# Kernel optimization log

Measured on AMD Instinct MI355X. Metric: run time of the kernel, lower is better.

## Reference

```python
import jax, jax.numpy as jnp
import numpy as np

B, S, D, H = 4, 2048, 1024, 16


def setup_inputs() -> dict:
    key = jax.random.key(0)
    ks = jax.random.split(key, 5)
    scale = 1.0 / np.sqrt(D)
    return {
        "q": jax.random.normal(ks[0], (B, S, D), jnp.float32),
        "v": jax.random.normal(ks[1], (B, S, D), jnp.float32),
        "Wq": jax.random.normal(ks[2], (D, D), jnp.float32) * scale,
        "bq": jnp.zeros((D,), jnp.float32),
        "Wk": jax.random.normal(ks[3], (D, D), jnp.float32) * scale,
        "bk": jnp.zeros((D,), jnp.float32),
        "Wv": jax.random.normal(ks[4], (D, D), jnp.float32) * scale,
        "bv": jnp.zeros((D,), jnp.float32),
    }


def reference(q, v, Wq, bq, Wk, bk, Wv, bv):
    # k defaults to v in the original call
    k = v
    embed_dim = Wq.shape[0]
    num_heads = H
    dh = embed_dim // num_heads
    b, s, _ = q.shape

    qp = q @ Wq + bq  # [B,S,D]
    kp = k @ Wk + bk
    vp = v @ Wv + bv

    # tf.split(x, H, axis=2) + concat on axis 0 == reshape to [B,S,H,dh]
    qh = qp.reshape(b, s, num_heads, dh)
    kh = kp.reshape(b, s, num_heads, dh)
    vh = vp.reshape(b, s, num_heads, dh)

    # NOTE: original scales by sqrt(embed_dim), NOT sqrt(head_dim)
    scores = jnp.einsum("bqhd,bkhd->bhqk", qh, kh) / jnp.sqrt(
        jnp.asarray(embed_dim, qh.dtype)
    )
    att = jax.nn.softmax(scores, axis=-1)
    out = jnp.einsum("bhqk,bkhd->bqhd", att, vh)
    return out.reshape(b, s, embed_dim)
```

## Files before the change

kernel.cpp:

```cpp
#include <hip/hip_runtime.h>
#include <hip/hip_bf16.h>
#include <math.h>

#define B_   4
#define S_   2048
#define D_   1024
#define H_   16
#define DH_  64
#define M_   (B_ * S_)
#define BH_  (B_ * H_)

typedef __bf16 bf16x8_t __attribute__((ext_vector_type(8)));
typedef float  f32x4_t  __attribute__((ext_vector_type(4)));
typedef float  f32x16_t __attribute__((ext_vector_type(16)));

#define QSCALE 0.045084220027780106f

__device__ __forceinline__ unsigned short f2bf(float x) {
  unsigned int u = __float_as_uint(x);
  u += 0x7fffu + ((u >> 16) & 1u);
  return (unsigned short)(u >> 16);
}

__device__ __forceinline__ unsigned int pk2t(float lo, float hi) {
  return __builtin_amdgcn_perm(__float_as_uint(hi), __float_as_uint(lo), 0x07060302u);
}

__device__ __forceinline__ void async16(const void* g, void* l) {
  __builtin_amdgcn_global_load_lds(
      (__attribute__((address_space(1))) unsigned int*)(void*)g,
      (__attribute__((address_space(3))) unsigned int*)l, 16, 0, 0);
}

__global__ __launch_bounds__(256) void cvt_f32_bf16(
    const float* __restrict__ q, const float* __restrict__ v,
    unsigned short* __restrict__ qb, unsigned short* __restrict__ vb) {
  const float* src = blockIdx.y ? v : q;
  unsigned short* dst = blockIdx.y ? vb : qb;
  size_t i = ((size_t)blockIdx.x * 256 + threadIdx.x) * 4;
  float4 a = *(const float4*)(src + i);
  ushort4 o;
  o.x = f2bf(a.x); o.y = f2bf(a.y); o.z = f2bf(a.z); o.w = f2bf(a.w);
  *(ushort4*)(dst + i) = o;
}

__global__ void wtrans(const float* __restrict__ Wq, const float* __restrict__ Wk,
                       const float* __restrict__ Wv,
                       unsigned short* __restrict__ Wqt, unsigned short* __restrict__ Wkt,
                       unsigned short* __restrict__ Wvt) {
  int z = blockIdx.z;
  const float* W = (z == 0) ? Wq : (z == 1 ? Wk : Wv);
  unsigned short* Wt = (z == 0) ? Wqt : (z == 1 ? Wkt : Wvt);
  __shared__ float tile[32][33];
  int tx = threadIdx.x, ty = threadIdx.y;
  int n = blockIdx.x * 32 + tx;
#pragma unroll
  for (int i = 0; i < 4; ++i) {
    int k = blockIdx.y * 32 + ty + i * 8;
    tile[ty + i * 8][tx] = W[(size_t)k * D_ + n];
  }
  __syncthreads();
  int k2 = blockIdx.y * 32 + tx;
#pragma unroll
  for (int i = 0; i < 4; ++i) {
    int n2 = blockIdx.x * 32 + ty + i * 8;
    Wt[(size_t)n2 * D_ + k2] = f2bf(tile[tx][ty + i * 8]);
  }
}

__global__ __launch_bounds__(256) void proj_gemm(
    const unsigned short* __restrict__ Aq, const unsigned short* __restrict__ Av,
    const unsigned short* __restrict__ Wqt, const unsigned short* __restrict__ Wkt,
    const unsigned short* __restrict__ Wvt,
    const float* __restrict__ bq, const float* __restrict__ bk, const float* __restrict__ bv,
    unsigned short* __restrict__ qp, unsigned short* __restrict__ kp,
    unsigned short* __restrict__ vt) {
  int z = blockIdx.y;
  const unsigned short* A  = (z == 0) ? Aq : Av;
  const unsigned short* Wt = (z == 0) ? Wqt : (z == 1 ? Wkt : Wvt);
  const float* bias        = (z == 0) ? bq : (z == 1 ? bk : bv);
  unsigned short* outp     = (z == 0) ? qp : (z == 1 ? kp : vt);
  const float cs           = (z == 0) ? QSCALE : 1.0f;

  int lin = blockIdx.x;
  int xcd = lin & 7, j = lin >> 3;
  int m0 = (xcd * 8 + (j & 7)) * 128;
  int n0 = (j >> 3) * 128;

  __shared__ __attribute__((aligned(16))) unsigned short Alds[128 * 32];
  __shared__ __attribute__((aligned(16))) unsigned short Blds[128 * 32];

  int t = threadIdx.x;
  int lane = t & 63, wave = t >> 6;
  int lrow = lane & 15, lq = lane >> 4;
  int wm = (wave & 1) * 64, wn = (wave >> 1) * 64;

  f32x4_t acc[4][4];
#pragma unroll
  for (int i = 0; i < 4; ++i)
#pragma unroll
    for (int j2 = 0; j2 < 4; ++j2) acc[i][j2] = (f32x4_t){0.f, 0.f, 0.f, 0.f};

  for (int k0 = 0; k0 < D_; k0 += 32) {
    __syncthreads();
#pragma unroll
    for (int r = 0; r < 2; ++r) {
      int off = t * 16 + r * 4096;
      int row = off >> 6, slot = (off >> 4) & 3;
      int ch = (slot ^ (row >> 1)) & 3;
      async16((const char*)A  + ((size_t)(m0 + row) * D_ + k0) * 2 + ch * 16, (char*)Alds + off);
      async16((const char*)Wt + ((size_t)(n0 + row) * D_ + k0) * 2 + ch * 16, (char*)Blds + off);
    }
    __syncthreads();

    bf16x8_t af[4], bfr[4];
#pragma unroll
    for (int i = 0; i < 4; ++i) {
      int ra = wm + i * 16 + lrow;
      int rb = wn + i * 16 + lrow;
      af[i]  = *(const bf16x8_t*)(Alds + ra * 32 + ((lq ^ (ra >> 1)) & 3) * 8);
      bfr[i] = *(const bf16x8_t*)(Blds + rb * 32 + ((lq ^ (rb >> 1)) & 3) * 8);
    }
#pragma unroll
    for (int i = 0; i < 4; ++i)
#pragma unroll
      for (int j2 = 0; j2 < 4; ++j2)
        acc[i][j2] = __builtin_amdgcn_mfma_f32_16x16x32_bf16(af[i], bfr[j2], acc[i][j2], 0, 0, 0);
  }

#pragma unroll
  for (int j2 = 0; j2 < 4; ++j2) {
    int n = n0 + wn + j2 * 16 + lrow;
    float bv_ = bias[n];
    int h = n >> 6, d = n & 63;
#pragma unroll
    for (int i = 0; i < 4; ++i) {
      int mbase = m0 + wm + i * 16 + lq * 4;
      int b = mbase >> 11, s = mbase & 2047;
      if (z != 2) {
#pragma unroll
        for (int r = 0; r < 4; ++r)
          outp[(((size_t)(b * H_ + h) * S_ + (s + r)) << 6) + d] = f2bf((acc[i][j2][r] + bv_) * cs);
      } else {
        ushort4 pk;
        pk.x = f2bf(acc[i][j2][0] + bv_);
        pk.y = f2bf(acc[i][j2][1] + bv_);
        pk.z = f2bf(acc[i][j2][2] + bv_);
        pk.w = f2bf(acc[i][j2][3] + bv_);
        *(ushort4*)(outp + (((size_t)(b * H_ + h) * 64 + d) << 11) + s) = pk;
      }
    }
  }
}

__global__ __launch_bounds__(256, 2) void attn(
    const unsigned short* __restrict__ qp, const unsigned short* __restrict__ kp,
    const unsigned short* __restrict__ vt, float* __restrict__ out) {
  const int bh = blockIdx.x;
  const int qt = blockIdx.y;
  const int t = threadIdx.x;
  const int lane = t & 63, wave = t >> 6;
  const int h = lane >> 5, ln = lane & 31;

  __shared__ __attribute__((aligned(16))) unsigned short Klds[2][64 * 64];
  __shared__ __attribute__((aligned(16))) unsigned short Vlds[2][64 * 64];

  const int q0 = qt * 256 + wave * 64;

  bf16x8_t qf[2][4];
#pragma unroll
  for (int rt = 0; rt < 2; ++rt)
#pragma unroll
    for (int ks = 0; ks < 4; ++ks)
      qf[rt][ks] = *(const bf16x8_t*)(qp + ((size_t)bh * S_ + q0 + rt * 32 + ln) * 64 + ks * 16 + h * 8);

  f32x16_t o[2][2];
  float l[2] = {0.f, 0.f};
#pragma unroll
  for (int rt = 0; rt < 2; ++rt)
#pragma unroll
    for (int dt = 0; dt < 2; ++dt)
#pragma unroll
      for (int r = 0; r < 16; ++r) o[rt][dt][r] = 0.f;

  f32x16_t z16;
#pragma unroll
  for (int r = 0; r < 16; ++r) z16[r] = 0.f;

  const unsigned short* kg = kp + (size_t)bh * S_ * 64;
  const unsigned short* vg = vt + (size_t)bh * 64 * S_;

  auto stage = [&](int kb, int bi) {
#pragma unroll
    for (int r = 0; r < 2; ++r) {
      int off = t * 16 + r * 4096;
      int row = off >> 7, slot = (off >> 4) & 7;
      int ch = slot ^ (row & 7);
      async16((const char*)(kg + (size_t)(kb + row) * 64 + ch * 8), (char*)&Klds[bi][0] + off);
      async16((const char*)(vg + (size_t)row * S_ + kb + ch * 8), (char*)&Vlds[bi][0] + off);
    }
  };

  stage(0, 0);

  const int NT = S_ / 64;
  for (int it = 0; it < NT; ++it) {
    const int bi = it & 1;
    __syncthreads();
    if (it + 1 < NT) stage((it + 1) * 64, bi ^ 1);

    const unsigned short* Kb = &Klds[bi][0];
    const unsigned short* Vb = &Vlds[bi][0];

    f32x16_t st[2][2];
#pragma unroll
    for (int kt = 0; kt < 2; ++kt) {
      {
        int row = kt * 32 + ln;
        bf16x8_t kf = *(const bf16x8_t*)(Kb + row * 64 + (((0 + h) ^ (row & 7)) * 8));
        st[0][kt] = __builtin_amdgcn_mfma_f32_32x32x16_bf16(kf, qf[0][0], z16, 0, 0, 0);
        st[1][kt] = __builtin_amdgcn_mfma_f32_32x32x16_bf16(kf, qf[1][0], z16, 0, 0, 0);
      }
#pragma unroll
      for (int ks = 1; ks < 4; ++ks) {
        int row = kt * 32 + ln;
        bf16x8_t kf = *(const bf16x8_t*)(Kb + row * 64 + (((ks * 2 + h) ^ (row & 7)) * 8));
        st[0][kt] = __builtin_amdgcn_mfma_f32_32x32x16_bf16(kf, qf[0][ks], st[0][kt], 0, 0, 0);
        st[1][kt] = __builtin_amdgcn_mfma_f32_32x32x16_bf16(kf, qf[1][ks], st[1][kt], 0, 0, 0);
      }
    }

    unsigned int pkv[2][2][8];
#pragma unroll
    for (int rt = 0; rt < 2; ++rt) {
      float lp = 0.f;
#pragma unroll
      for (int kt = 0; kt < 2; ++kt)
#pragma unroll
        for (int i = 0; i < 8; ++i) {
          float p0 = __builtin_amdgcn_exp2f(st[rt][kt][2 * i]);
          float p1 = __builtin_amdgcn_exp2f(st[rt][kt][2 * i + 1]);
          lp += p0 + p1;
          pkv[rt][kt][i] = pk2t(p0, p1);
        }
      l[rt] += lp + __shfl_xor(lp, 32);
    }

    bf16x8_t pf[2][4];
#pragma unroll
    for (int rt = 0; rt < 2; ++rt)
#pragma unroll
      for (int ks = 0; ks < 4; ++ks) {
        int kt = ks >> 1, b = 4 * (ks & 1);
        unsigned int e0 = __shfl_xor(h ? pkv[rt][kt][b]     : pkv[rt][kt][b + 2], 32);
        unsigned int e1 = __shfl_xor(h ? pkv[rt][kt][b + 1] : pkv[rt][kt][b + 3], 32);
        union { unsigned int u[4]; bf16x8_t v; } fr;
        fr.u[0] = h ? e0 : pkv[rt][kt][b];
        fr.u[1] = h ? e1 : pkv[rt][kt][b + 1];
        fr.u[2] = h ? pkv[rt][kt][b + 2] : e0;
        fr.u[3] = h ? pkv[rt][kt][b + 3] : e1;
        pf[rt][ks] = fr.v;
      }

#pragma unroll
    for (int dt = 0; dt < 2; ++dt)
#pragma unroll
      for (int ks = 0; ks < 4; ++ks) {
        int row = dt * 32 + ln;
        bf16x8_t vf = *(const bf16x8_t*)(Vb + row * 64 + (((ks * 2 + h) ^ (row & 7)) * 8));
#pragma unroll
        for (int rt = 0; rt < 2; ++rt)
          o[rt][dt] = __builtin_amdgcn_mfma_f32_32x32x16_bf16(pf[rt][ks], vf, o[rt][dt], 0, 0, 0);
      }
  }

  const int b = bh >> 4, head = bh & 15;
#pragma unroll
  for (int rt = 0; rt < 2; ++rt)
#pragma unroll
    for (int r = 0; r < 16; ++r) {
      int rowl = (r & 3) + 8 * (r >> 2) + 4 * h;
      float li = __shfl(l[rt], rowl, 64);
      float inv = __builtin_amdgcn_rcpf(li);
      int rg = q0 + rt * 32 + rowl;
      float* op = out + ((size_t)b * S_ + rg) * D_ + head * 64 + ln;
      op[0]  = o[rt][0][r] * inv;
      op[32] = o[rt][1][r] * inv;
    }
}

extern "C" void kernel_launch(void* const* d_in, const int* in_sizes, int n_in,
                              void* d_out, int out_size, void* d_ws, size_t ws_size,
                              hipStream_t stream) {
  const float* q  = (const float*)d_in[0];
  const float* v  = (const float*)d_in[1];
  const float* Wq = (const float*)d_in[2];
  const float* bq = (const float*)d_in[3];
  const float* Wk = (const float*)d_in[4];
  const float* bk = (const float*)d_in[5];
  const float* Wv = (const float*)d_in[6];
  const float* bv = (const float*)d_in[7];
  float* out = (float*)d_out;

  char* ws = (char*)d_ws;
  unsigned short* qb  = (unsigned short*)(ws);
  unsigned short* vb  = (unsigned short*)(ws + (16u << 20));
  unsigned short* Wqt = (unsigned short*)(ws + (32u << 20));
  unsigned short* Wkt = (unsigned short*)(ws + (34u << 20));
  unsigned short* Wvt = (unsigned short*)(ws + (36u << 20));
  unsigned short* qpp = (unsigned short*)(ws + (38u << 20));
  unsigned short* kpp = (unsigned short*)(ws + (54u << 20));
  unsigned short* vtp = (unsigned short*)(ws + (70u << 20));

  hipLaunchKernelGGL(cvt_f32_bf16, dim3((M_ * D_) / 1024, 2), dim3(256), 0, stream,
                     q, v, qb, vb);
  hipLaunchKernelGGL(wtrans, dim3(32, 32, 3), dim3(32, 8), 0, stream,
                     Wq, Wk, Wv, Wqt, Wkt, Wvt);
  hipLaunchKernelGGL(proj_gemm, dim3(512, 3), dim3(256), 0, stream,
                     qb, vb, Wqt, Wkt, Wvt, bq, bk, bv, qpp, kpp, vtp);
  hipLaunchKernelGGL(attn, dim3(BH_, S_ / 256), dim3(256), 0, stream,
                     qpp, kpp, vtp, out);
}
```

Baseline: 274.3 us.

## Deepen projection GEMM K-tile, shrink attention query tile, compute row sums via MFMA

The projection GEMM now stages 64-wide K slices with an 8-chunk XOR swizzle, which halves the number of barrier-separated loop iterations. The attention kernel drops from 64 to 32 query rows per wave and doubles the grid. It raises launch bounds to 4 blocks per CU so more waves can hide latency. The softmax denominator now comes from an extra MFMA against a ones vector instead of scalar adds and shuffles. This adds MFMA work and halves K/V reuse per staged tile, trading that for lower register pressure and higher occupancy.

```diff
diff --git a/kernel.cpp b/kernel.cpp
--- a/kernel.cpp
+++ b/kernel.cpp
@@ -87,8 +87,8 @@
   int m0 = (xcd * 8 + (j & 7)) * 128;
   int n0 = (j >> 3) * 128;
 
-  __shared__ __attribute__((aligned(16))) unsigned short Alds[128 * 32];
-  __shared__ __attribute__((aligned(16))) unsigned short Blds[128 * 32];
+  __shared__ __attribute__((aligned(16))) unsigned short Alds[128 * 64];
+  __shared__ __attribute__((aligned(16))) unsigned short Blds[128 * 64];
 
   int t = threadIdx.x;
   int lane = t & 63, wave = t >> 6;
@@ -101,31 +101,34 @@
 #pragma unroll
     for (int j2 = 0; j2 < 4; ++j2) acc[i][j2] = (f32x4_t){0.f, 0.f, 0.f, 0.f};
 
-  for (int k0 = 0; k0 < D_; k0 += 32) {
+  for (int k0 = 0; k0 < D_; k0 += 64) {
     __syncthreads();
 #pragma unroll
-    for (int r = 0; r < 2; ++r) {
+    for (int r = 0; r < 4; ++r) {
       int off = t * 16 + r * 4096;
-      int row = off >> 6, slot = (off >> 4) & 3;
-      int ch = (slot ^ (row >> 1)) & 3;
+      int row = off >> 7, slot = (off >> 4) & 7;
+      int ch = slot ^ (row & 7);
       async16((const char*)A  + ((size_t)(m0 + row) * D_ + k0) * 2 + ch * 16, (char*)Alds + off);
       async16((const char*)Wt + ((size_t)(n0 + row) * D_ + k0) * 2 + ch * 16, (char*)Blds + off);
     }
     __syncthreads();
 
-    bf16x8_t af[4], bfr[4];
-#pragma unroll
-    for (int i = 0; i < 4; ++i) {
-      int ra = wm + i * 16 + lrow;
-      int rb = wn + i * 16 + lrow;
-      af[i]  = *(const bf16x8_t*)(Alds + ra * 32 + ((lq ^ (ra >> 1)) & 3) * 8);
-      bfr[i] = *(const bf16x8_t*)(Blds + rb * 32 + ((lq ^ (rb >> 1)) & 3) * 8);
-    }
-#pragma unroll
-    for (int i = 0; i < 4; ++i)
-#pragma unroll
-      for (int j2 = 0; j2 < 4; ++j2)
-        acc[i][j2] = __builtin_amdgcn_mfma_f32_16x16x32_bf16(af[i], bfr[j2], acc[i][j2], 0, 0, 0);
+#pragma unroll
+    for (int kk = 0; kk < 2; ++kk) {
+      bf16x8_t af[4], bfr[4];
+#pragma unroll
+      for (int i = 0; i < 4; ++i) {
+        int ra = wm + i * 16 + lrow;
+        int rb = wn + i * 16 + lrow;
+        af[i]  = *(const bf16x8_t*)((const char*)Alds + ra * 128 + (((lq + 4 * kk) ^ (ra & 7)) * 16));
+        bfr[i] = *(const bf16x8_t*)((const char*)Blds + rb * 128 + (((lq + 4 * kk) ^ (rb & 7)) * 16));
+      }
+#pragma unroll
+      for (int i = 0; i < 4; ++i)
+#pragma unroll
+        for (int j2 = 0; j2 < 4; ++j2)
+          acc[i][j2] = __builtin_amdgcn_mfma_f32_16x16x32_bf16(af[i], bfr[j2], acc[i][j2], 0, 0, 0);
+    }
   }
 
 #pragma unroll
@@ -153,7 +156,7 @@
   }
 }
 
-__global__ __launch_bounds__(256, 2) void attn(
+__global__ __launch_bounds__(256, 4) void attn(
     const unsigned short* __restrict__ qp, const unsigned short* __restrict__ kp,
     const unsigned short* __restrict__ vt, float* __restrict__ out) {
   const int bh = blockIdx.x;
@@ -165,27 +168,25 @@
   __shared__ __attribute__((aligned(16))) unsigned short Klds[2][64 * 64];
   __shared__ __attribute__((aligned(16))) unsigned short Vlds[2][64 * 64];
 
-  const int q0 = qt * 256 + wave * 64;
-
-  bf16x8_t qf[2][4];
-#pragma unroll
-  for (int rt = 0; rt < 2; ++rt)
-#pragma unroll
-    for (int ks = 0; ks < 4; ++ks)
-      qf[rt][ks] = *(const bf16x8_t*)(qp + ((size_t)bh * S_ + q0 + rt * 32 + ln) * 64 + ks * 16 + h * 8);
-
-  f32x16_t o[2][2];
-  float l[2] = {0.f, 0.f};
-#pragma unroll
-  for (int rt = 0; rt < 2; ++rt)
-#pragma unroll
-    for (int dt = 0; dt < 2; ++dt)
-#pragma unroll
-      for (int r = 0; r < 16; ++r) o[rt][dt][r] = 0.f;
+  const int q0 = qt * 128 + wave * 32;
+
+  bf16x8_t qf[4];
+#pragma unroll
+  for (int ks = 0; ks < 4; ++ks)
+    qf[ks] = *(const bf16x8_t*)(qp + ((size_t)bh * S_ + q0 + ln) * 64 + ks * 16 + h * 8);
+
+  f32x16_t o[2];
+  f32x16_t o_l;
+#pragma unroll
+  for (int r = 0; r < 16; ++r) { o[0][r] = 0.f; o[1][r] = 0.f; o_l[r] = 0.f; }
 
   f32x16_t z16;
 #pragma unroll
   for (int r = 0; r < 16; ++r) z16[r] = 0.f;
+
+  bf16x8_t onesf;
+#pragma unroll
+  for (int i = 0; i < 8; ++i) onesf[i] = (__bf16)1.0f;
 
   const unsigned short* kg = kp + (size_t)bh * S_ * 64;
   const unsigned short* vg = vt + (size_t)bh * 64 * S_;
@@ -212,81 +213,70 @@
     const unsigned short* Kb = &Klds[bi][0];
     const unsigned short* Vb = &Vlds[bi][0];
 
-    f32x16_t st[2][2];
+    f32x16_t st[2];
 #pragma unroll
     for (int kt = 0; kt < 2; ++kt) {
+      int row = kt * 32 + ln;
       {
-        int row = kt * 32 + ln;
-        bf16x8_t kf = *(const bf16x8_t*)(Kb + row * 64 + (((0 + h) ^ (row & 7)) * 8));
-        st[0][kt] = __builtin_amdgcn_mfma_f32_32x32x16_bf16(kf, qf[0][0], z16, 0, 0, 0);
-        st[1][kt] = __builtin_amdgcn_mfma_f32_32x32x16_bf16(kf, qf[1][0], z16, 0, 0, 0);
+        bf16x8_t kf = *(const bf16x8_t*)(Kb + row * 64 + ((h ^ (row & 7)) * 8));
+        st[kt] = __builtin_amdgcn_mfma_f32_32x32x16_bf16(kf, qf[0], z16, 0, 0, 0);
       }
 #pragma unroll
       for (int ks = 1; ks < 4; ++ks) {
-        int row = kt * 32 + ln;
         bf16x8_t kf = *(const bf16x8_t*)(Kb + row * 64 + (((ks * 2 + h) ^ (row & 7)) * 8));
-        st[0][kt] = __builtin_amdgcn_mfma_f32_32x32x16_bf16(kf, qf[0][ks], st[0][kt], 0, 0, 0);
-        st[1][kt] = __builtin_amdgcn_mfma_f32_32x32x16_bf16(kf, qf[1][ks], st[1][kt], 0, 0, 0);
-      }
-    }
-
-    unsigned int pkv[2][2][8];
-#pragma unroll
-    for (int rt = 0; rt < 2; ++rt) {
-      float lp = 0.f;
-#pragma unroll
-      for (int kt = 0; kt < 2; ++kt)
-#pragma unroll
-        for (int i = 0; i < 8; ++i) {
-          float p0 = __builtin_amdgcn_exp2f(st[rt][kt][2 * i]);
-          float p1 = __builtin_amdgcn_exp2f(st[rt][kt][2 * i + 1]);
-          lp += p0 + p1;
-          pkv[rt][kt][i] = pk2t(p0, p1);
-        }
-      l[rt] += lp + __shfl_xor(lp, 32);
-    }
-
-    bf16x8_t pf[2][4];
-#pragma unroll
-    for (int rt = 0; rt < 2; ++rt)
+        st[kt] = __builtin_amdgcn_mfma_f32_32x32x16_bf16(kf, qf[ks], st[kt], 0, 0, 0);
+      }
+    }
+
+    unsigned int pkv[2][8];
+#pragma unroll
+    for (int kt = 0; kt < 2; ++kt)
+#pragma unroll
+      for (int i = 0; i < 8; ++i) {
+        float p0 = __builtin_amdgcn_exp2f(st[kt][2 * i]);
+        float p1 = __builtin_amdgcn_exp2f(st[kt][2 * i + 1]);
+        pkv[kt][i] = pk2t(p0, p1);
+      }
+
+    bf16x8_t pf[4];
+#pragma unroll
+    for (int ks = 0; ks < 4; ++ks) {
+      int kt = ks >> 1, b = 4 * (ks & 1);
+      unsigned int e0 = __shfl_xor(h ? pkv[kt][b]     : pkv[kt][b + 2], 32);
+      unsigned int e1 = __shfl_xor(h ? pkv[kt][b + 1] : pkv[kt][b + 3], 32);
+      union { unsigned int u[4]; bf16x8_t v; } fr;
+      fr.u[0] = h ? e0 : pkv[kt][b];
+      fr.u[1] = h ? e1 : pkv[kt][b + 1];
+      fr.u[2] = h ? pkv[kt][b + 2] : e0;
+      fr.u[3] = h ? pkv[kt][b + 3] : e1;
+      pf[ks] = fr.v;
+    }
+
+#pragma unroll
+    for (int ks = 0; ks < 4; ++ks)
+      o_l = __builtin_amdgcn_mfma_f32_32x32x16_bf16(pf[ks], onesf, o_l, 0, 0, 0);
+
+#pragma unroll
+    for (int dt = 0; dt < 2; ++dt) {
+      int row = dt * 32 + ln;
 #pragma unroll
       for (int ks = 0; ks < 4; ++ks) {
-        int kt = ks >> 1, b = 4 * (ks & 1);
-        unsigned int e0 = __shfl_xor(h ? pkv[rt][kt][b]     : pkv[rt][kt][b + 2], 32);
-        unsigned int e1 = __shfl_xor(h ? pkv[rt][kt][b + 1] : pkv[rt][kt][b + 3], 32);
-        union { unsigned int u[4]; bf16x8_t v; } fr;
-        fr.u[0] = h ? e0 : pkv[rt][kt][b];
-        fr.u[1] = h ? e1 : pkv[rt][kt][b + 1];
-        fr.u[2] = h ? pkv[rt][kt][b + 2] : e0;
-        fr.u[3] = h ? pkv[rt][kt][b + 3] : e1;
-        pf[rt][ks] = fr.v;
-      }
-
-#pragma unroll
-    for (int dt = 0; dt < 2; ++dt)
-#pragma unroll
-      for (int ks = 0; ks < 4; ++ks) {
-        int row = dt * 32 + ln;
         bf16x8_t vf = *(const bf16x8_t*)(Vb + row * 64 + (((ks * 2 + h) ^ (row & 7)) * 8));
-#pragma unroll
-        for (int rt = 0; rt < 2; ++rt)
-          o[rt][dt] = __builtin_amdgcn_mfma_f32_32x32x16_bf16(pf[rt][ks], vf, o[rt][dt], 0, 0, 0);
-      }
+        o[dt] = __builtin_amdgcn_mfma_f32_32x32x16_bf16(pf[ks], vf, o[dt], 0, 0, 0);
+      }
+    }
   }
 
   const int b = bh >> 4, head = bh & 15;
 #pragma unroll
-  for (int rt = 0; rt < 2; ++rt)
-#pragma unroll
-    for (int r = 0; r < 16; ++r) {
-      int rowl = (r & 3) + 8 * (r >> 2) + 4 * h;
-      float li = __shfl(l[rt], rowl, 64);
-      float inv = __builtin_amdgcn_rcpf(li);
-      int rg = q0 + rt * 32 + rowl;
-      float* op = out + ((size_t)b * S_ + rg) * D_ + head * 64 + ln;
-      op[0]  = o[rt][0][r] * inv;
-      op[32] = o[rt][1][r] * inv;
-    }
+  for (int r = 0; r < 16; ++r) {
+    int rowl = (r & 3) + 8 * (r >> 2) + 4 * h;
+    float inv = __builtin_amdgcn_rcpf(o_l[r]);
+    int rg = q0 + rowl;
+    float* op = out + ((size_t)b * S_ + rg) * D_ + head * 64 + ln;
+    op[0]  = o[0][r] * inv;
+    op[32] = o[1][r] * inv;
+  }
 }
 
 extern "C" void kernel_launch(void* const* d_in, const int* in_sizes, int n_in,
@@ -318,6 +308,6 @@
                      Wq, Wk, Wv, Wqt, Wkt, Wvt);
   hipLaunchKernelGGL(proj_gemm, dim3(512, 3), dim3(256), 0, stream,
                      qb, vb, Wqt, Wkt, Wvt, bq, bk, bv, qpp, kpp, vtp);
-  hipLaunchKernelGGL(attn, dim3(BH_, S_ / 256), dim3(256), 0, stream,
+  hipLaunchKernelGGL(attn, dim3(BH_, S_ / 128), dim3(256), 0, stream,
                      qpp, kpp, vtp, out);
 }
```

Result: no change. 279.1 us (+1.8%).
